# Kernel optimization log

Measured on AMD Instinct MI355X. Metric: run time of the kernel, lower is better.

## Reference

```python
import jax, jax.numpy as jnp
import numpy as np

NEG_SLOPE = 0.2
K_L = 0.5
K_G = 0.5
TEMP_G = 1e-3


def _leaky(v):
    return jnp.where(v >= 0, v, NEG_SLOPE * v)


def _topk_row_mask(scores, keep):
    # scores: [n, n, h]; torch.topk(dim=0) -> indices [keep, n] per head,
    # then head_mask[indices, :] = 1 selects whole ROWS (any column hit).
    n = scores.shape[0]
    s = jnp.transpose(scores, (1, 2, 0))        # [n_cols, h, n_rows]
    _, idx = jax.lax.top_k(s, keep)             # [n_cols, h, keep]

    def per_head(idx_h):                        # idx_h: [n_cols, keep]
        return jnp.zeros((n,), scores.dtype).at[idx_h.reshape(-1)].set(1.0)

    rows = jax.vmap(per_head, in_axes=1, out_axes=0)(idx)  # [h, n_rows]
    return jnp.transpose(rows)[:, None, :]      # [n_rows, 1, h] broadcast over cols


def setup_inputs() -> dict:
    key = jax.random.key(0)
    ks = jax.random.split(key, 8)
    n, in_f, feat_dim = 1024, 256, 128
    H, F = 4, 64                                # n_heads, n_hidden (out_features=256)
    feats = jax.random.normal(ks[0], (n, feat_dim), dtype=jnp.float32)
    x = jax.random.normal(ks[1], (n, in_f), dtype=jnp.float32)
    adj = jax.random.randint(ks[2], (n, n, 1), 0, 2).astype(jnp.int32)
    sc = 0.05
    W_l = jax.random.normal(ks[3], (in_f, H * F), dtype=jnp.float32) * sc
    W_r = jax.random.normal(ks[4], (in_f, H * F), dtype=jnp.float32) * sc
    attn_w = jax.random.normal(ks[5], (F,), dtype=jnp.float32) * sc
    W_delta = jax.random.normal(ks[6], (2 * F, F), dtype=jnp.float32) * sc
    b_delta = jnp.zeros((F,), dtype=jnp.float32)
    return {"feats": feats, "x": x, "adj": adj, "W_l": W_l, "W_r": W_r,
            "attn_w": attn_w, "W_delta": W_delta, "b_delta": b_delta}


def reference(feats, x, adj, W_l, W_r, attn_w, W_delta, b_delta):
    n = x.shape[0]
    F = attn_w.shape[0]
    H = W_l.shape[1] // F
    g_l = (x @ W_l).reshape(n, H, F)
    g_r = (x @ W_r).reshape(n, H, F)
    # g_sum[i, j] = g_l[j] + g_r[i]  (repeat vs repeat_interleave ordering)
    g_sum = g_r[:, None, :, :] + g_l[None, :, :, :]          # [n, n, H, F]
    e = jnp.einsum('ijhf,f->ijh', _leaky(g_sum), attn_w)     # [n, n, H]

    mask_adj = adj > 0                                        # [n, n, 1]
    a_l = jax.nn.softmax(jnp.where(mask_adj, e, -jnp.inf), axis=1)
    a_1nd = a_l * mask_adj.astype(e.dtype)

    keep_l = int(n * (1.0 - K_L))
    a_filt = a_1nd * _topk_row_mask(a_1nd, keep_l)
    attn_local = jnp.einsum('ijh,jhf->ihf', a_filt, g_r)     # [n, H, F]

    omega = jax.nn.softmax(e, axis=1)
    fn = (feats - feats.min(axis=0)) / (feats.max(axis=0) - feats.min(axis=0))
    fn = jnp.where(jnp.isnan(fn), 0.0, fn)
    g_rn = (g_r - g_r.min(axis=0)) / (g_r.max(axis=0) - g_r.min(axis=0))
    nf = jnp.linalg.norm(fn, axis=1)                          # [n] (index j)
    ng = jnp.linalg.norm(g_rn, axis=2)                        # [n, H] (index i)
    alpha = jax.nn.softmax(jnp.abs(nf[None, :, None] - ng[:, None, :]), axis=1)
    gamma = 0.5 * (omega + (1.0 - alpha))

    keep_g = int(n * (1.0 - K_G))
    gf = gamma * _topk_row_mask(gamma, keep_g)
    gf = jax.nn.softmax(jnp.where(gf == 0, 1e-10, gf) / TEMP_G, axis=1)
    attn_global = jnp.einsum('ijh,jhf->ihf', gf, g_r)         # [n, H, F]

    inter = _leaky(jnp.concatenate([attn_local, attn_global], axis=2) @ W_delta + b_delta)
    delta = jax.nn.softmax(inter, axis=1)                     # softmax over heads (torch dim=1)
    attn_res = delta * attn_local + (1.0 - delta) * attn_global
    return attn_res.reshape(n, H * F)
```

## Files before the change

kernel.cpp:

```cpp
#include <hip/hip_runtime.h>
#include <cstdint>
#include <cstddef>

#define N 1024
#define HN 4
#define FDIM 64
#define KSEL 512
#define FLT_MAX_ 3.402823466e+38f

__device__ __forceinline__ float wred_sum(float v){
#pragma unroll
  for(int o=32;o>0;o>>=1) v += __shfl_down(v,o,64);
  return v;
}
__device__ __forceinline__ float bfly_sum(float v){
#pragma unroll
  for(int o=1;o<64;o<<=1) v += __shfl_xor(v,o,64);
  return v;
}
__device__ __forceinline__ float bfly_max(float v){
#pragma unroll
  for(int o=1;o<64;o<<=1) v = fmaxf(v,__shfl_xor(v,o,64));
  return v;
}
__device__ __forceinline__ float bred_sum(float v, float* scr){
  int t=threadIdx.x;
  v = wred_sum(v);
  __syncthreads();
  if((t&63)==0) scr[t>>6]=v;
  __syncthreads();
  return (scr[0]+scr[1])+(scr[2]+scr[3]);
}

__global__ __launch_bounds__(256) void stage1(const float* __restrict__ x,
                                              const float* __restrict__ W_l,
                                              const float* __restrict__ W_r,
                                              const int* __restrict__ adj,
                                              const float* __restrict__ feats,
                                              float* __restrict__ g_l,
                                              float* __restrict__ g_r,
                                              unsigned* __restrict__ adjbit,
                                              int* __restrict__ masks,
                                              float* __restrict__ pmin_f,
                                              float* __restrict__ pmax_f){
  int bx = blockIdx.x, t = threadIdx.x;
  if(bx < 512){
    const float* __restrict__ W = (bx >= 256) ? W_r : W_l;
    float* __restrict__ g = (bx >= 256) ? g_r : g_l;
    int i0 = (bx & 255)*4;
    float acc[4] = {0.f,0.f,0.f,0.f};
#pragma unroll 8
    for(int k=0;k<256;k++){
      float w = W[(size_t)k*256 + t];
#pragma unroll
      for(int r=0;r<4;r++) acc[r] = fmaf(x[(size_t)(i0+r)*256 + k], w, acc[r]);
    }
#pragma unroll
    for(int r=0;r<4;r++) g[(size_t)(i0+r)*256 + t] = acc[r];
  } else if(bx < 1536){
    int i = bx - 512, w = t>>6, lane = t&63;
    if(i < 32) masks[i*256 + t] = 0;
#pragma unroll
    for(int it=0; it<4; it++){
      int j = w*256 + it*64 + lane;
      int v = adj[(size_t)i*N + j];
      unsigned long long mb = __ballot(v > 0);
      if(lane == 0){
        adjbit[i*32 + w*8 + it*2]     = (unsigned)mb;
        adjbit[i*32 + w*8 + it*2 + 1] = (unsigned)(mb >> 32);
      }
    }
  } else {
    int chunk = bx - 1536;
    if(t < 128){
      float lo = FLT_MAX_, hi = -FLT_MAX_;
      int r0 = chunk*64;
      for(int r=0;r<64;r++){
        float v = feats[(size_t)(r0+r)*128 + t];
        lo = fminf(lo,v); hi = fmaxf(hi,v);
      }
      pmin_f[chunk*128+t]=lo; pmax_f[chunk*128+t]=hi;
    }
  }
}

__global__ __launch_bounds__(256) void stage2(const float* __restrict__ g_l,
                                              const float* __restrict__ g_r,
                                              const float* __restrict__ attn_w,
                                              const float* __restrict__ feats,
                                              const float* __restrict__ pmin_f, const float* __restrict__ pmax_f,
                                              float* __restrict__ pmin_g, float* __restrict__ pmax_g,
                                              float* __restrict__ psum_g,
                                              float* __restrict__ nf,
                                              float* __restrict__ e,
                                              float* __restrict__ eT){
  __shared__ __align__(16) float smem[2*64*68 + 128];
  int bx = blockIdx.x, t = threadIdx.x;
  if(bx < 1024){
    float* grs = smem;
    float* gls = smem + 64*68;
    float* aw  = smem + 2*64*68;
    float* aw2 = aw + 64;
    int h = bx >> 8, i0 = ((bx>>4)&15)*64, j0 = (bx&15)*64;
    if(t < 64){ float w = attn_w[t]; aw[t]=w; aw2[t]=0.2f*w; }
#pragma unroll
    for(int k=0;k<16;k++){
      int idx = t + k*256; int r = idx>>6, f = idx&63;
      grs[r*68+f] = g_r[(size_t)(i0+r)*256 + h*64 + f];
      gls[r*68+f] = g_l[(size_t)(j0+r)*256 + h*64 + f];
    }
    __syncthreads();
    int tj = t&15, ti = t>>4;
    float acc[4][4];
#pragma unroll
    for(int a=0;a<4;a++)
#pragma unroll
      for(int b=0;b<4;b++) acc[a][b]=0.f;
    for(int fc=0; fc<64; fc+=4){
      float4 wv  = *(float4*)&aw[fc];
      float4 wv2 = *(float4*)&aw2[fc];
      float4 ga4[4], gb4[4];
#pragma unroll
      for(int a=0;a<4;a++) ga4[a] = *(float4*)&grs[(ti*4+a)*68+fc];
#pragma unroll
      for(int b=0;b<4;b++) gb4[b] = *(float4*)&gls[(tj+16*b)*68+fc];
#pragma unroll
      for(int a=0;a<4;a++)
#pragma unroll
        for(int b=0;b<4;b++){
          float s0 = ga4[a].x + gb4[b].x;
          float s1 = ga4[a].y + gb4[b].y;
          float s2 = ga4[a].z + gb4[b].z;
          float s3 = ga4[a].w + gb4[b].w;
          acc[a][b] = fmaf(s0, (s0>=0.f)?wv.x:wv2.x, acc[a][b]);
          acc[a][b] = fmaf(s1, (s1>=0.f)?wv.y:wv2.y, acc[a][b]);
          acc[a][b] = fmaf(s2, (s2>=0.f)?wv.z:wv2.z, acc[a][b]);
          acc[a][b] = fmaf(s3, (s3>=0.f)?wv.w:wv2.w, acc[a][b]);
        }
    }
#pragma unroll
    for(int a=0;a<4;a++)
#pragma unroll
      for(int b=0;b<4;b++){
        int i = i0 + ti*4 + a, j = j0 + tj + 16*b;
        e[((size_t)h*N + i)*N + j] = acc[a][b];
      }
    __syncthreads();
    float* esT = smem;
#pragma unroll
    for(int a=0;a<4;a++)
#pragma unroll
      for(int b=0;b<4;b++)
        esT[(tj + 16*b)*68 + ti*4 + a] = acc[a][b];
    __syncthreads();
#pragma unroll
    for(int k=0;k<4;k++){
      int jl = (t>>4) + 16*k, ilx = (t&15)*4;
      *(float4*)(eT + ((size_t)h*N + j0 + jl)*N + i0 + ilx) = *(float4*)&esT[jl*68 + ilx];
    }
  } else if(bx < 1040){
    int chunk = bx - 1024;
    float lo = FLT_MAX_, hi = -FLT_MAX_, sm = 0.f;
    int r0 = chunk*64;
    for(int r=0;r<64;r++){
      float v = g_r[(size_t)(r0+r)*256 + t];
      lo = fminf(lo,v); hi = fmaxf(hi,v); sm += v;
    }
    pmin_g[chunk*256+t]=lo; pmax_g[chunk*256+t]=hi; psum_g[chunk*256+t]=sm;
  } else {
    int i = bx - 1040;
    float* scr = smem;
    float u = 0.f;
    if(t < 128){
      float lo = FLT_MAX_, hi = -FLT_MAX_;
#pragma unroll
      for(int k=0;k<16;k++){
        lo = fminf(lo, pmin_f[k*128+t]);
        hi = fmaxf(hi, pmax_f[k*128+t]);
      }
      float d = hi - lo;
      float v = feats[(size_t)i*128 + t];
      u = (d==0.f) ? 0.f : (v - lo)/d;
    }
    float tot = bred_sum(u*u, scr);
    if(t==0) nf[i] = sqrtf(tot);
  }
}

__global__ __launch_bounds__(256) void row_stats(const float* __restrict__ e,
                                                 const unsigned* __restrict__ adjbit,
                                                 const float* __restrict__ nf,
                                                 const float* __restrict__ g_r,
                                                 const float* __restrict__ pmin_g, const float* __restrict__ pmax_g,
                                                 float* __restrict__ ng,
                                                 float* __restrict__ mlA, float* __restrict__ islA,
                                                 float* __restrict__ moA, float* __restrict__ isoA,
                                                 float* __restrict__ maA, float* __restrict__ isaA,
                                                 float* __restrict__ mgA, float* __restrict__ sgA){
  int i = blockIdx.x, t = threadIdx.x, h = t>>6, lane = t&63;
  float glo = FLT_MAX_, ghi = -FLT_MAX_;
#pragma unroll
  for(int k=0;k<16;k++){
    glo = fminf(glo, pmin_g[k*256 + h*64 + lane]);
    ghi = fmaxf(ghi, pmax_g[k*256 + h*64 + lane]);
  }
  float dg = ghi - glo;
  float ug = (g_r[(size_t)i*256 + h*64 + lane] - glo)/dg;
  float ngv = sqrtf(bfly_sum(ug*ug));
  if(lane==0) ng[h*N + i] = ngv;

  size_t base = ((size_t)h*N + i)*N;
  float er[16], nfr[16];
  unsigned nib[4];
#pragma unroll
  for(int c=0;c<4;c++){
    float4 e4 = *(const float4*)(e  + base + c*256 + lane*4);
    float4 n4 = *(const float4*)(nf + c*256 + lane*4);
    er[c*4+0]=e4.x; er[c*4+1]=e4.y; er[c*4+2]=e4.z; er[c*4+3]=e4.w;
    nfr[c*4+0]=n4.x; nfr[c*4+1]=n4.y; nfr[c*4+2]=n4.z; nfr[c*4+3]=n4.w;
    nib[c] = (adjbit[i*32 + c*8 + (lane>>3)] >> ((lane&7)*4)) & 0xFu;
  }
  float ml=-FLT_MAX_, mo=-FLT_MAX_, ma=-FLT_MAX_;
#pragma unroll
  for(int c=0;c<4;c++)
#pragma unroll
    for(int k=0;k<4;k++){
      int q = c*4+k;
      float ev = er[q];
      mo = fmaxf(mo, ev);
      if((nib[c]>>k)&1) ml = fmaxf(ml, ev);
      ma = fmaxf(ma, fabsf(nfr[q]-ngv));
    }
  ml = bfly_max(ml); mo = bfly_max(mo); ma = bfly_max(ma);
  float sl=0.f, so=0.f, sa=0.f;
#pragma unroll
  for(int c=0;c<4;c++)
#pragma unroll
    for(int k=0;k<4;k++){
      int q = c*4+k;
      float ev = er[q];
      so += __expf(ev-mo);
      if((nib[c]>>k)&1) sl += __expf(ev-ml);
      sa += __expf(fabsf(nfr[q]-ngv)-ma);
    }
  sl = bfly_sum(sl); so = bfly_sum(so); sa = bfly_sum(sa);
  float isl = 1.f/sl, iso = 1.f/so, isa = 1.f/sa;
  float gg[16];
  float mg = -FLT_MAX_;
#pragma unroll
  for(int q=0;q<16;q++){
    float ev = er[q];
    float omega = __expf(ev-mo)*iso;
    float alpha = __expf(fabsf(nfr[q]-ngv)-ma)*isa;
    float g = 0.5f*(omega + 1.f - alpha);
    gg[q] = g;
    mg = fmaxf(mg, g);
  }
  mg = bfly_max(mg);
  float sg = 0.f;
#pragma unroll
  for(int q=0;q<16;q++) sg += __expf((gg[q]-mg)/1e-3f);
  sg = bfly_sum(sg);
  if(lane==0){
    mlA[h*N+i]=ml; islA[h*N+i]=isl;
    moA[h*N+i]=mo; isoA[h*N+i]=iso;
    maA[h*N+i]=ma; isaA[h*N+i]=isa;
    mgA[h*N+i]=mg; sgA[h*N+i]=sg;
  }
}

__device__ __forceinline__ void apply_mask(const unsigned* ur, unsigned T, int tneed, int EQ,
                                           int* __restrict__ mask, int base, int lane){
  if(EQ == tneed){
#pragma unroll
    for(int c=0;c<4;c++)
#pragma unroll
      for(int k2=0;k2<4;k2++){
        int i = c*256 + lane*4 + k2;
        if(ur[c*4+k2] >= T) mask[base + i] = 1;
      }
  } else {
    int run_base = 0;
#pragma unroll
    for(int c=0;c<4;c++){
      unsigned long long bm[4];
#pragma unroll
      for(int k2=0;k2<4;k2++) bm[k2] = __ballot(ur[c*4+k2]==T);
      unsigned long long lower = (lane==0) ? 0ull : (~0ull >> (64-lane));
      int run = run_base;
#pragma unroll
      for(int k2=0;k2<4;k2++) run += (int)__popcll(bm[k2] & lower);
#pragma unroll
      for(int k2=0;k2<4;k2++){
        int i = c*256 + lane*4 + k2;
        unsigned u = ur[c*4+k2];
        bool sel = (u > T) || (u == T && run < tneed);
        run += (u==T)?1:0;
        if(sel) mask[base + i] = 1;
      }
      int ctot = 0;
#pragma unroll
      for(int k2=0;k2<4;k2++) ctot += (int)__popcll(bm[k2]);
      run_base += ctot;
    }
  }
}

__global__ __launch_bounds__(256) void mm_sel(const float* __restrict__ eT,
                                              const float* __restrict__ g_r,
                                              const unsigned* __restrict__ adjbit,
                                              const float* __restrict__ nf,
                                              const float* __restrict__ mlA, const float* __restrict__ islA,
                                              const float* __restrict__ moA, const float* __restrict__ isoA,
                                              const float* __restrict__ maA, const float* __restrict__ isaA,
                                              const float* __restrict__ ngA,
                                              const float* __restrict__ mgA, const float* __restrict__ sgA,
                                              float* __restrict__ partL,
                                              float* __restrict__ partG,
                                              int* __restrict__ mask_l,
                                              int* __restrict__ mask_g){
  __shared__ __align__(16) float a_t[2][32][36];
  __shared__ __align__(16) float p_t[2][32][36];
  __shared__ __align__(16) float b_s[2][32][68];
  int bx = blockIdx.x, h = blockIdx.y, s = blockIdx.z;
  int t = threadIdx.x;

  if(bx >= 32){
    int w = t>>6, lane = t&63;
    int sid = (bx - 32) + 64*(h + 4*s);
    int gcol = sid*4 + w;
    int z  = gcol >> 12;
    int hj = gcol & 4095;
    int hh = hj >> 10, jc = hj & 1023;
    const float* __restrict__ src = eT + (size_t)hj * (size_t)N;

    float ev[16];
#pragma unroll
    for(int c=0;c<4;c++){
      float4 e4 = ((const float4*)src)[c*64 + lane];
      ev[c*4+0]=e4.x; ev[c*4+1]=e4.y; ev[c*4+2]=e4.z; ev[c*4+3]=e4.w;
    }
    unsigned ur[16];
    if(z == 0){
      int wo = jc >> 5; unsigned bm = 1u << (jc & 31);
#pragma unroll
      for(int c=0;c<4;c++){
        int ib = (hh<<10) + c*256 + lane*4;
        float4 ml4 = *(const float4*)(mlA+ib);
        float4 il4 = *(const float4*)(islA+ib);
        float mlv[4] = {ml4.x,ml4.y,ml4.z,ml4.w};
        float ilv[4] = {il4.x,il4.y,il4.z,il4.w};
#pragma unroll
        for(int k=0;k<4;k++){
          int i = c*256 + lane*4 + k;
          float a = (adjbit[i*32 + wo] & bm) ? __expf(ev[c*4+k]-mlv[k])*ilv[k] : 0.f;
          ur[c*4+k] = __float_as_uint(a);
        }
      }
    } else {
      float nfv = nf[jc];
#pragma unroll
      for(int c=0;c<4;c++){
        int ib = (hh<<10) + c*256 + lane*4;
        float4 mo4 = *(const float4*)(moA+ib);
        float4 io4 = *(const float4*)(isoA+ib);
        float4 ma4 = *(const float4*)(maA+ib);
        float4 ia4 = *(const float4*)(isaA+ib);
        float4 ng4 = *(const float4*)(ngA+ib);
        float mov[4]={mo4.x,mo4.y,mo4.z,mo4.w}, iov[4]={io4.x,io4.y,io4.z,io4.w};
        float mav[4]={ma4.x,ma4.y,ma4.z,ma4.w}, iav[4]={ia4.x,ia4.y,ia4.z,ia4.w};
        float ngv[4]={ng4.x,ng4.y,ng4.z,ng4.w};
#pragma unroll
        for(int k=0;k<4;k++){
          float omega = __expf(ev[c*4+k]-mov[k])*iov[k];
          float alpha = __expf(fabsf(nfv-ngv[k])-mav[k])*iav[k];
          float g = 0.5f*(omega + 1.f - alpha);
          ur[c*4+k] = __float_as_uint(g);
        }
      }
    }

    unsigned prefix = 0u;
    for(int b=30; b>=0; b--){
      unsigned cand = prefix | (1u<<b);
      int c = 0;
#pragma unroll
      for(int q=0;q<16;q++) c += (int)__popcll(__ballot(ur[q] >= cand));
      prefix = (c >= KSEL) ? cand : prefix;
    }
    unsigned T = prefix;
    int GT = 0, EQ = 0;
#pragma unroll
    for(int q=0;q<16;q++){
      GT += (int)__popcll(__ballot(ur[q] > T));
      EQ += (int)__popcll(__ballot(ur[q] == T));
    }
    int tneed = KSEL - GT;

    int* __restrict__ mask = z ? mask_g : mask_l;
    apply_mask(ur, T, tneed, EQ, mask, hh<<10, lane);
    return;
  }

  int i0 = bx*32, j0 = s*128;
  int il = t & 31, jq = t >> 5;
  int gi = h*N + i0 + il;
  float ml_r = mlA[gi], il_r = islA[gi];
  float mo_r = moA[gi], io_r = isoA[gi];
  float ma_r = maA[gi], ia_r = isaA[gi];
  float ng_r = ngA[gi];
  float mg_r = mgA[gi], isg_r = 1.f/sgA[gi];
  int fq = t & 15, iq = t >> 4;
  int jb2a = t>>4, d4a = t&15;
  int idxb = t + 256, jb2b = idxb>>4, d4b = idxb&15;

  float e0,e1,e2,e3; unsigned aw; float4 nf4, vb0, vb1;
  {
    int jb = j0;
    size_t ebase = ((size_t)h*N + jb + jq*4)*(size_t)N + i0 + il;
    e0 = eT[ebase]; e1 = eT[ebase+N]; e2 = eT[ebase+2*N]; e3 = eT[ebase+3*N];
    aw = adjbit[(size_t)(i0+il)*32 + s*4 + 0];
    nf4 = *(const float4*)(nf + jb + jq*4);
    vb0 = *(const float4*)(g_r + (size_t)(jb+jb2a)*256 + h*64 + d4a*4);
    vb1 = *(const float4*)(g_r + (size_t)(jb+jb2b)*256 + h*64 + d4b*4);
  }
  {
    float evs[4] = {e0,e1,e2,e3};
    float nfsv[4] = {nf4.x,nf4.y,nf4.z,nf4.w};
#pragma unroll
    for(int c=0;c<4;c++){
      int jl = jq*4 + c;
      float a = ((aw >> jl) & 1u) ? __expf(evs[c]-ml_r)*il_r : 0.f;
      float omega = __expf(evs[c]-mo_r)*io_r;
      float alpha = __expf(fabsf(nfsv[c]-ng_r)-ma_r)*ia_r;
      float g = 0.5f*(omega + 1.f - alpha);
      float p = __expf((g-mg_r)/1e-3f)*isg_r;
      a_t[0][jl][il] = a;
      p_t[0][jl][il] = p;
    }
    *(float4*)&b_s[0][jb2a][d4a*4] = vb0;
    *(float4*)&b_s[0][jb2b][d4b*4] = vb1;
  }
  float4 accL[2], accG[2];
#pragma unroll
  for(int r=0;r<2;r++){ accL[r]=make_float4(0,0,0,0); accG[r]=make_float4(0,0,0,0); }

  for(int sub=0; sub<4; sub++){
    int cur = sub & 1;
    __syncthreads();
    if(sub < 3){
      int jb = j0 + (sub+1)*32;
      size_t ebase = ((size_t)h*N + jb + jq*4)*(size_t)N + i0 + il;
      e0 = eT[ebase]; e1 = eT[ebase+N]; e2 = eT[ebase+2*N]; e3 = eT[ebase+3*N];
      aw = adjbit[(size_t)(i0+il)*32 + s*4 + sub + 1];
      nf4 = *(const float4*)(nf + jb + jq*4);
      vb0 = *(const float4*)(g_r + (size_t)(jb+jb2a)*256 + h*64 + d4a*4);
      vb1 = *(const float4*)(g_r + (size_t)(jb+jb2b)*256 + h*64 + d4b*4);
    }
#pragma unroll 8
    for(int j=0;j<32;j++){
      float4 bv = *(float4*)&b_s[cur][j][fq*4];
      float2 av = *(float2*)&a_t[cur][j][iq*2];
      float2 pv = *(float2*)&p_t[cur][j][iq*2];
      accL[0].x = fmaf(av.x, bv.x, accL[0].x); accL[0].y = fmaf(av.x, bv.y, accL[0].y);
      accL[0].z = fmaf(av.x, bv.z, accL[0].z); accL[0].w = fmaf(av.x, bv.w, accL[0].w);
      accL[1].x = fmaf(av.y, bv.x, accL[1].x); accL[1].y = fmaf(av.y, bv.y, accL[1].y);
      accL[1].z = fmaf(av.y, bv.z, accL[1].z); accL[1].w = fmaf(av.y, bv.w, accL[1].w);
      accG[0].x = fmaf(pv.x, bv.x, accG[0].x); accG[0].y = fmaf(pv.x, bv.y, accG[0].y);
      accG[0].z = fmaf(pv.x, bv.z, accG[0].z); accG[0].w = fmaf(pv.x, bv.w, accG[0].w);
      accG[1].x = fmaf(pv.y, bv.x, accG[1].x); accG[1].y = fmaf(pv.y, bv.y, accG[1].y);
      accG[1].z = fmaf(pv.y, bv.z, accG[1].z); accG[1].w = fmaf(pv.y, bv.w, accG[1].w);
    }
    if(sub < 3){
      int nxt = 1 - cur;
      float evs[4] = {e0,e1,e2,e3};
      float nfsv[4] = {nf4.x,nf4.y,nf4.z,nf4.w};
#pragma unroll
      for(int c=0;c<4;c++){
        int jl = jq*4 + c;
        float a = ((aw >> jl) & 1u) ? __expf(evs[c]-ml_r)*il_r : 0.f;
        float omega = __expf(evs[c]-mo_r)*io_r;
        float alpha = __expf(fabsf(nfsv[c]-ng_r)-ma_r)*ia_r;
        float g = 0.5f*(omega + 1.f - alpha);
        float p = __expf((g-mg_r)/1e-3f)*isg_r;
        a_t[nxt][jl][il] = a;
        p_t[nxt][jl][il] = p;
      }
      *(float4*)&b_s[nxt][jb2a][d4a*4] = vb0;
      *(float4*)&b_s[nxt][jb2b][d4b*4] = vb1;
    }
  }
#pragma unroll
  for(int r=0;r<2;r++){
    int i = i0 + iq*2 + r;
    size_t o = ((size_t)s*N + i)*256 + h*64 + fq*4;
    *(float4*)&partL[o] = accL[r];
    *(float4*)&partG[o] = accG[r];
  }
}

__global__ __launch_bounds__(256) void epilogue(const float* __restrict__ partL,
                                                const float* __restrict__ partG,
                                                const int* __restrict__ mask_l,
                                                const int* __restrict__ mask_g,
                                                const float* __restrict__ psum_g,
                                                const float* __restrict__ W_delta,
                                                const float* __restrict__ b_delta,
                                                float* __restrict__ out){
  __shared__ float cat[4][128];
  __shared__ float inter_s[4][64];
  int i = blockIdx.x, t = threadIdx.x;
  int h = t>>6, f = t&63;
  float sl = 0.f, sg = 0.f;
#pragma unroll
  for(int s2=0;s2<8;s2++){
    size_t o = ((size_t)s2*N + i)*256 + h*64 + f;
    sl += partL[o];
    sg += partG[o];
  }
  if(!mask_l[h*N + i]) sl = 0.f;
  if(!mask_g[h*N + i]){
    float gs = 0.f;
#pragma unroll
    for(int k=0;k<16;k++) gs += psum_g[k*256 + t];
    sg = gs * (1.f/1024.f);
  }
  cat[h][f]      = sl;
  cat[h][64 + f] = sg;
  __syncthreads();
  float d = b_delta[f];
  for(int c=0;c<128;c++) d = fmaf(cat[h][c], W_delta[(size_t)c*64 + f], d);
  d = (d >= 0.f) ? d : 0.2f*d;
  inter_s[h][f] = d;
  __syncthreads();
  float m = inter_s[0][f];
#pragma unroll
  for(int hh=1;hh<4;hh++) m = fmaxf(m, inter_s[hh][f]);
  float ssum = 0.f;
#pragma unroll
  for(int hh=0;hh<4;hh++) ssum += __expf(inter_s[hh][f]-m);
  float delta = __expf(d - m)/ssum;
  out[(size_t)i*256 + h*64 + f] = delta*sl + (1.f - delta)*sg;
}

extern "C" void kernel_launch(void* const* d_in, const int* in_sizes, int n_in,
                              void* d_out, int out_size, void* d_ws, size_t ws_size,
                              hipStream_t stream) {
  const float* feats  = (const float*)d_in[0];
  const float* x      = (const float*)d_in[1];
  const int*   adj    = (const int*)  d_in[2];
  const float* W_l    = (const float*)d_in[3];
  const float* W_r    = (const float*)d_in[4];
  const float* attn_w = (const float*)d_in[5];
  const float* W_delta= (const float*)d_in[6];
  const float* b_delta= (const float*)d_in[7];
  float* out = (float*)d_out;

  float* ws = (float*)d_ws;
  size_t off = 0;
  float* g_l   = ws+off; off += (size_t)N*256;
  float* g_r   = ws+off; off += (size_t)N*256;
  float* e     = ws+off; off += (size_t)HN*N*N;
  float* eT    = ws+off; off += (size_t)HN*N*N;
  float* partL = ws+off; off += (size_t)8*N*256;
  float* partG = ws+off; off += (size_t)8*N*256;
  float* pmin_f= ws+off; off += 16*128;
  float* pmax_f= ws+off; off += 16*128;
  float* pmin_g= ws+off; off += 16*256;
  float* pmax_g= ws+off; off += 16*256;
  float* psum_g= ws+off; off += 16*256;
  float* nf    = ws+off; off += N;
  float* ng    = ws+off; off += (size_t)HN*N;
  float* mlA   = ws+off; off += (size_t)HN*N;
  float* islA  = ws+off; off += (size_t)HN*N;
  float* moA   = ws+off; off += (size_t)HN*N;
  float* isoA  = ws+off; off += (size_t)HN*N;
  float* maA   = ws+off; off += (size_t)HN*N;
  float* isaA  = ws+off; off += (size_t)HN*N;
  float* mgA   = ws+off; off += (size_t)HN*N;
  float* sgA   = ws+off; off += (size_t)HN*N;
  int* mask_l  = (int*)(ws+off); off += (size_t)HN*N;
  int* mask_g  = (int*)(ws+off); off += (size_t)HN*N;
  unsigned* adjbit = (unsigned*)(ws+off); off += (size_t)N*32;

  stage1<<<1552, 256, 0, stream>>>(x, W_l, W_r, adj, feats, g_l, g_r, adjbit, mask_l, pmin_f, pmax_f);

  stage2<<<2064, 256, 0, stream>>>(g_l, g_r, attn_w, feats, pmin_f, pmax_f,
                                   pmin_g, pmax_g, psum_g, nf, e, eT);

  row_stats<<<N, 256, 0, stream>>>(e, adjbit, nf, g_r, pmin_g, pmax_g, ng,
                                   mlA, islA, moA, isoA, maA, isaA, mgA, sgA);

  mm_sel<<<dim3(96,HN,8), 256, 0, stream>>>(eT, g_r, adjbit, nf,
                                            mlA, islA, moA, isoA, maA, isaA, ng,
                                            mgA, sgA, partL, partG, mask_l, mask_g);

  epilogue<<<N, 256, 0, stream>>>(partL, partG, mask_l, mask_g, psum_g, W_delta, b_delta, out);
}
```

Baseline: 181.2 us.

## Halve j-split in mm_sel, single-buffer LDS, merge local/global selection per wave

```diff
diff --git a/kernel.cpp b/kernel.cpp
--- a/kernel.cpp
+++ b/kernel.cpp
@@ -306,6 +306,27 @@
   }
 }
 
+__device__ __forceinline__ void run_select(const unsigned* ur, int* __restrict__ mask,
+                                           int base, int lane){
+  unsigned prefix = 0u;
+  for(int b=30; b>=0; b--){
+    unsigned cand = prefix | (1u<<b);
+    int c = 0;
+#pragma unroll
+    for(int q=0;q<16;q++) c += (int)__popcll(__ballot(ur[q] >= cand));
+    prefix = (c >= KSEL) ? cand : prefix;
+  }
+  unsigned T = prefix;
+  int GT = 0, EQ = 0;
+#pragma unroll
+  for(int q=0;q<16;q++){
+    GT += (int)__popcll(__ballot(ur[q] > T));
+    EQ += (int)__popcll(__ballot(ur[q] == T));
+  }
+  int tneed = KSEL - GT;
+  apply_mask(ur, T, tneed, EQ, mask, base, lane);
+}
+
 __global__ __launch_bounds__(256) void mm_sel(const float* __restrict__ eT,
                                               const float* __restrict__ g_r,
                                               const unsigned* __restrict__ adjbit,
@@ -319,9 +340,9 @@
                                               float* __restrict__ partG,
                                               int* __restrict__ mask_l,
                                               int* __restrict__ mask_g){
-  __shared__ __align__(16) float a_t[2][32][36];
-  __shared__ __align__(16) float p_t[2][32][36];
-  __shared__ __align__(16) float b_s[2][32][68];
+  __shared__ __align__(16) float a_t[32][36];
+  __shared__ __align__(16) float p_t[32][36];
+  __shared__ __align__(16) float b_s[32][68];
   int bx = blockIdx.x, h = blockIdx.y, s = blockIdx.z;
   int t = threadIdx.x;
 
@@ -329,10 +350,8 @@
     int w = t>>6, lane = t&63;
     int sid = (bx - 32) + 64*(h + 4*s);
     int gcol = sid*4 + w;
-    int z  = gcol >> 12;
-    int hj = gcol & 4095;
-    int hh = hj >> 10, jc = hj & 1023;
-    const float* __restrict__ src = eT + (size_t)hj * (size_t)N;
+    int hh = gcol >> 10, jc = gcol & 1023;
+    const float* __restrict__ src = eT + (size_t)gcol * (size_t)N;
 
     float ev[16];
 #pragma unroll
@@ -341,7 +360,7 @@
       ev[c*4+0]=e4.x; ev[c*4+1]=e4.y; ev[c*4+2]=e4.z; ev[c*4+3]=e4.w;
     }
     unsigned ur[16];
-    if(z == 0){
+    {
       int wo = jc >> 5; unsigned bm = 1u << (jc & 31);
 #pragma unroll
       for(int c=0;c<4;c++){
@@ -357,7 +376,9 @@
           ur[c*4+k] = __float_as_uint(a);
         }
       }
-    } else {
+      run_select(ur, mask_l, hh<<10, lane);
+    }
+    {
       float nfv = nf[jc];
 #pragma unroll
       for(int c=0;c<4;c++){
@@ -378,31 +399,12 @@
           ur[c*4+k] = __float_as_uint(g);
         }
       }
-    }
-
-    unsigned prefix = 0u;
-    for(int b=30; b>=0; b--){
-      unsigned cand = prefix | (1u<<b);
-      int c = 0;
-#pragma unroll
-      for(int q=0;q<16;q++) c += (int)__popcll(__ballot(ur[q] >= cand));
-      prefix = (c >= KSEL) ? cand : prefix;
-    }
-    unsigned T = prefix;
-    int GT = 0, EQ = 0;
-#pragma unroll
-    for(int q=0;q<16;q++){
-      GT += (int)__popcll(__ballot(ur[q] > T));
-      EQ += (int)__popcll(__ballot(ur[q] == T));
-    }
-    int tneed = KSEL - GT;
-
-    int* __restrict__ mask = z ? mask_g : mask_l;
-    apply_mask(ur, T, tneed, EQ, mask, hh<<10, lane);
+      run_select(ur, mask_g, hh<<10, lane);
+    }
     return;
   }
 
-  int i0 = bx*32, j0 = s*128;
+  int i0 = bx*32, j0 = s*256;
   int il = t & 31, jq = t >> 5;
   int gi = h*N + i0 + il;
   float ml_r = mlA[gi], il_r = islA[gi];
@@ -419,49 +421,49 @@
     int jb = j0;
     size_t ebase = ((size_t)h*N + jb + jq*4)*(size_t)N + i0 + il;
     e0 = eT[ebase]; e1 = eT[ebase+N]; e2 = eT[ebase+2*N]; e3 = eT[ebase+3*N];
-    aw = adjbit[(size_t)(i0+il)*32 + s*4 + 0];
+    aw = adjbit[(size_t)(i0+il)*32 + s*8 + 0];
     nf4 = *(const float4*)(nf + jb + jq*4);
     vb0 = *(const float4*)(g_r + (size_t)(jb+jb2a)*256 + h*64 + d4a*4);
     vb1 = *(const float4*)(g_r + (size_t)(jb+jb2b)*256 + h*64 + d4b*4);
   }
-  {
-    float evs[4] = {e0,e1,e2,e3};
-    float nfsv[4] = {nf4.x,nf4.y,nf4.z,nf4.w};
-#pragma unroll
-    for(int c=0;c<4;c++){
-      int jl = jq*4 + c;
-      float a = ((aw >> jl) & 1u) ? __expf(evs[c]-ml_r)*il_r : 0.f;
-      float omega = __expf(evs[c]-mo_r)*io_r;
-      float alpha = __expf(fabsf(nfsv[c]-ng_r)-ma_r)*ia_r;
-      float g = 0.5f*(omega + 1.f - alpha);
-      float p = __expf((g-mg_r)/1e-3f)*isg_r;
-      a_t[0][jl][il] = a;
-      p_t[0][jl][il] = p;
-    }
-    *(float4*)&b_s[0][jb2a][d4a*4] = vb0;
-    *(float4*)&b_s[0][jb2b][d4b*4] = vb1;
-  }
   float4 accL[2], accG[2];
 #pragma unroll
   for(int r=0;r<2;r++){ accL[r]=make_float4(0,0,0,0); accG[r]=make_float4(0,0,0,0); }
 
-  for(int sub=0; sub<4; sub++){
-    int cur = sub & 1;
+  for(int sub=0; sub<8; sub++){
     __syncthreads();
-    if(sub < 3){
+    {
+      float evs[4] = {e0,e1,e2,e3};
+      float nfsv[4] = {nf4.x,nf4.y,nf4.z,nf4.w};
+#pragma unroll
+      for(int c=0;c<4;c++){
+        int jl = jq*4 + c;
+        float a = ((aw >> jl) & 1u) ? __expf(evs[c]-ml_r)*il_r : 0.f;
+        float omega = __expf(evs[c]-mo_r)*io_r;
+        float alpha = __expf(fabsf(nfsv[c]-ng_r)-ma_r)*ia_r;
+        float g = 0.5f*(omega + 1.f - alpha);
+        float p = __expf((g-mg_r)/1e-3f)*isg_r;
+        a_t[jl][il] = a;
+        p_t[jl][il] = p;
+      }
+      *(float4*)&b_s[jb2a][d4a*4] = vb0;
+      *(float4*)&b_s[jb2b][d4b*4] = vb1;
+    }
+    if(sub < 7){
       int jb = j0 + (sub+1)*32;
       size_t ebase = ((size_t)h*N + jb + jq*4)*(size_t)N + i0 + il;
       e0 = eT[ebase]; e1 = eT[ebase+N]; e2 = eT[ebase+2*N]; e3 = eT[ebase+3*N];
-      aw = adjbit[(size_t)(i0+il)*32 + s*4 + sub + 1];
+      aw = adjbit[(size_t)(i0+il)*32 + s*8 + sub + 1];
       nf4 = *(const float4*)(nf + jb + jq*4);
       vb0 = *(const float4*)(g_r + (size_t)(jb+jb2a)*256 + h*64 + d4a*4);
       vb1 = *(const float4*)(g_r + (size_t)(jb+jb2b)*256 + h*64 + d4b*4);
     }
+    __syncthreads();
 #pragma unroll 8
     for(int j=0;j<32;j++){
-      float4 bv = *(float4*)&b_s[cur][j][fq*4];
-      float2 av = *(float2*)&a_t[cur][j][iq*2];
-      float2 pv = *(float2*)&p_t[cur][j][iq*2];
+      float4 bv = *(float4*)&b_s[j][fq*4];
+      float2 av = *(float2*)&a_t[j][iq*2];
+      float2 pv = *(float2*)&p_t[j][iq*2];
       accL[0].x = fmaf(av.x, bv.x, accL[0].x); accL[0].y = fmaf(av.x, bv.y, accL[0].y);
       accL[0].z = fmaf(av.x, bv.z, accL[0].z); accL[0].w = fmaf(av.x, bv.w, accL[0].w);
       accL[1].x = fmaf(av.y, bv.x, accL[1].x); accL[1].y = fmaf(av.y, bv.y, accL[1].y);
@@ -470,24 +472,6 @@
       accG[0].z = fmaf(pv.x, bv.z, accG[0].z); accG[0].w = fmaf(pv.x, bv.w, accG[0].w);
       accG[1].x = fmaf(pv.y, bv.x, accG[1].x); accG[1].y = fmaf(pv.y, bv.y, accG[1].y);
       accG[1].z = fmaf(pv.y, bv.z, accG[1].z); accG[1].w = fmaf(pv.y, bv.w, accG[1].w);
-    }
-    if(sub < 3){
-      int nxt = 1 - cur;
-      float evs[4] = {e0,e1,e2,e3};
-      float nfsv[4] = {nf4.x,nf4.y,nf4.z,nf4.w};
-#pragma unroll
-      for(int c=0;c<4;c++){
-        int jl = jq*4 + c;
-        float a = ((aw >> jl) & 1u) ? __expf(evs[c]-ml_r)*il_r : 0.f;
-        float omega = __expf(evs[c]-mo_r)*io_r;
-        float alpha = __expf(fabsf(nfsv[c]-ng_r)-ma_r)*ia_r;
-        float g = 0.5f*(omega + 1.f - alpha);
-        float p = __expf((g-mg_r)/1e-3f)*isg_r;
-        a_t[nxt][jl][il] = a;
-        p_t[nxt][jl][il] = p;
-      }
-      *(float4*)&b_s[nxt][jb2a][d4a*4] = vb0;
-      *(float4*)&b_s[nxt][jb2b][d4b*4] = vb1;
     }
   }
 #pragma unroll
@@ -513,7 +497,7 @@
   int h = t>>6, f = t&63;
   float sl = 0.f, sg = 0.f;
 #pragma unroll
-  for(int s2=0;s2<8;s2++){
+  for(int s2=0;s2<4;s2++){
     size_t o = ((size_t)s2*N + i)*256 + h*64 + f;
     sl += partL[o];
     sg += partG[o];
@@ -562,8 +546,8 @@
   float* g_r   = ws+off; off += (size_t)N*256;
   float* e     = ws+off; off += (size_t)HN*N*N;
   float* eT    = ws+off; off += (size_t)HN*N*N;
-  float* partL = ws+off; off += (size_t)8*N*256;
-  float* partG = ws+off; off += (size_t)8*N*256;
+  float* partL = ws+off; off += (size_t)4*N*256;
+  float* partG = ws+off; off += (size_t)4*N*256;
   float* pmin_f= ws+off; off += 16*128;
   float* pmax_f= ws+off; off += 16*128;
   float* pmin_g= ws+off; off += 16*256;
@@ -591,7 +575,7 @@
   row_stats<<<N, 256, 0, stream>>>(e, adjbit, nf, g_r, pmin_g, pmax_g, ng,
                                    mlA, islA, moA, isoA, maA, isaA, mgA, sgA);
 
-  mm_sel<<<dim3(96,HN,8), 256, 0, stream>>>(eT, g_r, adjbit, nf,
+  mm_sel<<<dim3(96,HN,4), 256, 0, stream>>>(eT, g_r, adjbit, nf,
                                             mlA, islA, moA, isoA, maA, isaA, ng,
                                             mgA, sgA, partL, partG, mask_l, mask_g);
 
```

After: 184.6 us. Within noise of the previous version (+1.9%).
